# Performance work log

Hardware: AMD Instinct MI355X
Metric: run time of the kernel (lower is better)

The kernel has to match this reference:

```python
import jax, jax.numpy as jnp
import numpy as np

B, H, W, C = 32, 256, 256, 3
KH, KW, F = 5, 5, 8


def setup_inputs() -> dict:
    key = jax.random.key(0)
    k1, k2 = jax.random.split(key)
    x = jax.random.normal(k1, (B, H, W, C), dtype=jnp.float32)
    # learned structuring elements, shape (KH, KW, C, F) per build()
    kernel = jax.random.normal(k2, (KH, KW, C, F), dtype=jnp.float32) * 0.1
    return {"x": x, "kernel": kernel}


def _max_of_erosions(x, kernel):
    # tf.nn.erosion2d semantics: out[b,y,x,c] = min_{dy,dx} in[b, y+dy-pt, x+dx-pl, c]
    #                                               - kernel[KH-1-dy, KW-1-dx, c]
    # (erosion = -dilation(-x, reversed kernel)); then channel-max per filter.
    Bq, Hq, Wq, Cq = x.shape
    kh, kw, _, nf = kernel.shape
    pad_h, pad_w = kh - 1, kw - 1          # stride 1, rate 1, SAME padding
    pt, pl = pad_h // 2, pad_w // 2
    xp = jnp.pad(x, ((0, 0), (pt, pad_h - pt), (pl, pad_w - pl), (0, 0)),
                 constant_values=jnp.inf)   # +inf is identity for min
    kflip = kernel[::-1, ::-1]              # reflected structuring element
    ero = None                              # running min over window taps
    for dy in range(kh):                    # small fixed 5x5 tap loop
        for dx in range(kw):
            win = xp[:, dy:dy + Hq, dx:dx + Wq, :]          # [B,H,W,C]
            cand = win[..., None] - kflip[dy, dx]           # [B,H,W,C,F]
            ero = cand if ero is None else jnp.minimum(ero, cand)
    return jnp.max(ero, axis=3)             # channel max -> [B,H,W,F]


def reference(x, kernel):
    return _max_of_erosions(x, kernel)
```

## Files before the change

### kernel.cpp

```cpp
#include <hip/hip_runtime.h>
#include <math.h>


typedef _Float16 h2 __attribute__((ext_vector_type(2)));

static __device__ __forceinline__ h2 cvt_pk(float a, float b) {
    return __builtin_bit_cast(h2, __builtin_amdgcn_cvt_pkrtz(a, b));
}
static __device__ __forceinline__ h2 u2h(unsigned u) {
    return __builtin_bit_cast(h2, u);
}

#define Hq 256
#define RSTR 396
#define TILE_H2 (8 * RSTR)
#define INF2 0x7C007C00u

__global__ __launch_bounds__(256) void maxero_np(
    const float* __restrict__ x,
    const float* __restrict__ kern,
    float* __restrict__ out)
{
    __shared__ __align__(16) h2 xlds[TILE_H2];
    __shared__ __align__(16) h2 klds[25 * 12];

    const int tid = threadIdx.x;
    const int bI  = blockIdx.x;
    const int b   = bI >> 6;
    const int h0  = (bI & 63) << 2;

    for (int i = tid; i < 300; i += 256) {
        int tap = i / 12;
        int rem = i - tap * 12;
        int c = rem >> 2, fp = rem & 3;
        int dy = tap / 5, dx = tap - dy * 5;
        const float* kp = kern + (((4 - dy) * 5 + (4 - dx)) * 24) + c * 8 + fp * 2;
        klds[i] = cvt_pk(kp[0], kp[1]);
    }

    const float* xb = x + (size_t)b * (Hq * 256 * 3);
    #pragma unroll
    for (int k = 0; k < 6; ++k) {
        int chunk = tid + k * 256;
        int rr    = chunk / 192;
        int off   = (chunk - rr * 192) * 4;
        int r     = h0 - 2 + rr;
        bool rv   = (unsigned)r < (unsigned)Hq;
        int rc    = min(max(r, 0), Hq - 1);
        const float4 v = *reinterpret_cast<const float4*>(xb + rc * 768 + off);
        h2* d = &xlds[rr * RSTR + 9 + (off >> 1)];
        d[0] = rv ? cvt_pk(v.x, v.y) : u2h(INF2);
        d[1] = rv ? cvt_pk(v.z, v.w) : u2h(INF2);
    }
    if (tid < 96) {
        int rr = tid / 12, p = tid - rr * 12;
        xlds[rr * RSTR + (p < 9 ? p : 384 + p)] = u2h(INF2);
    }
    __syncthreads();

    const int hrow = tid >> 6;
    const int w0   = (tid & 63) << 2;

    h2 ero[4][3][4];
    #pragma unroll
    for (int p = 0; p < 4; ++p)
        #pragma unroll
        for (int c = 0; c < 3; ++c)
            #pragma unroll
            for (int fp = 0; fp < 4; ++fp)
                ero[p][c][fp] = u2h(INF2);

    #pragma unroll
    for (int dy = 0; dy < 5; ++dy) {
        const uint2* rp = reinterpret_cast<const uint2*>(
            &xlds[(hrow + dy) * RSTR + 6 + ((3 * w0) >> 1)]);
        unsigned nat[12];
        #pragma unroll
        for (int q = 0; q < 6; ++q) {
            uint2 t = rp[q];
            nat[q * 2 + 0] = t.x;
            nat[q * 2 + 1] = t.y;
        }
        #pragma unroll
        for (int dx = 0; dx < 5; ++dx) {
            const uint4* kk = reinterpret_cast<const uint4*>(&klds[(dy * 5 + dx) * 12]);
            uint4 k0 = kk[0], k1 = kk[1], k2 = kk[2];
            const unsigned kf[12] = { k0.x, k0.y, k0.z, k0.w,
                                      k1.x, k1.y, k1.z, k1.w,
                                      k2.x, k2.y, k2.z, k2.w };
            #pragma unroll
            for (int p = 0; p < 4; ++p)
                #pragma unroll
                for (int c = 0; c < 3; ++c) {
                    const int e = (p + dx) * 3 + c;
                    _Float16 s = u2h(nat[e >> 1])[e & 1];
                    h2 xx = { s, s };
                    #pragma unroll
                    for (int fp = 0; fp < 4; ++fp) {
                        h2 cand = xx - u2h(kf[c * 4 + fp]);
                        ero[p][c][fp] = __builtin_elementwise_min(ero[p][c][fp], cand);
                    }
                }
        }
    }

    const size_t rowbase = (size_t)b * 65536 + (size_t)(h0 + hrow) * 256 + w0;
    #pragma unroll
    for (int p = 0; p < 4; ++p) {
        float of[8];
        #pragma unroll
        for (int fp = 0; fp < 4; ++fp) {
            h2 m = __builtin_elementwise_max(
                       __builtin_elementwise_max(ero[p][0][fp], ero[p][1][fp]),
                       ero[p][2][fp]);
            of[fp * 2 + 0] = (float)m[0];
            of[fp * 2 + 1] = (float)m[1];
        }
        float* op = out + (rowbase + p) * 8;
        reinterpret_cast<float4*>(op)[0] = make_float4(of[0], of[1], of[2], of[3]);
        reinterpret_cast<float4*>(op)[1] = make_float4(of[4], of[5], of[6], of[7]);
    }
}

extern "C" void kernel_launch(void* const* d_in, const int* in_sizes, int n_in,
                              void* d_out, int out_size, void* d_ws, size_t ws_size,
                              hipStream_t stream) {
    const float* x    = (const float*)d_in[0];
    const float* kern = (const float*)d_in[1];
    float* out        = (float*)d_out;
    maxero_np<<<2048, 256, 0, stream>>>(x, kern, out);
}
```

Before: 53.97 us.

## Store input tile channel-planar so packed halves hold adjacent pixels

The shared-memory input tile moves from interleaved NHWC to per-channel planes, so each packed fp16 pair holds two neighbouring pixels of one channel. The kernel weights are now stored broadcast into both halves. Odd-offset pixel pairs are built with alignbit, so no per-element extract and broadcast is needed. This drops the scalar-to-vector splat work from the inner min loop. The cost is more LDS for the weights and a more involved global-to-LDS transpose.

```diff
diff --git a/kernel.cpp b/kernel.cpp
--- a/kernel.cpp
+++ b/kernel.cpp
@@ -12,114 +12,125 @@
 }
 
 #define Hq 256
-#define RSTR 396
-#define TILE_H2 (8 * RSTR)
+#define RST 132
+#define PST (8 * RST)
+#define TILE_H2 (3 * PST)
 #define INF2 0x7C007C00u
 
-__global__ __launch_bounds__(256) void maxero_np(
+__global__ __launch_bounds__(256) void maxero_pp(
     const float* __restrict__ x,
     const float* __restrict__ kern,
     float* __restrict__ out)
 {
-    __shared__ __align__(16) h2 xlds[TILE_H2];
-    __shared__ __align__(16) h2 klds[25 * 12];
+    __shared__ __align__(16) h2 xp[TILE_H2];
+    __shared__ __align__(16) h2 kd[600];
 
     const int tid = threadIdx.x;
     const int bI  = blockIdx.x;
     const int b   = bI >> 6;
     const int h0  = (bI & 63) << 2;
 
-    for (int i = tid; i < 300; i += 256) {
-        int tap = i / 12;
-        int rem = i - tap * 12;
-        int c = rem >> 2, fp = rem & 3;
+    for (int i = tid; i < 600; i += 256) {
+        int tap = i / 24, rem = i - tap * 24;
+        int c = rem >> 3, f = rem & 7;
         int dy = tap / 5, dx = tap - dy * 5;
-        const float* kp = kern + (((4 - dy) * 5 + (4 - dx)) * 24) + c * 8 + fp * 2;
-        klds[i] = cvt_pk(kp[0], kp[1]);
+        float v = kern[((4 - dy) * 5 + (4 - dx)) * 24 + c * 8 + f];
+        kd[i] = cvt_pk(v, v);
     }
 
     const float* xb = x + (size_t)b * (Hq * 256 * 3);
     #pragma unroll
-    for (int k = 0; k < 6; ++k) {
-        int chunk = tid + k * 256;
-        int rr    = chunk / 192;
-        int off   = (chunk - rr * 192) * 4;
-        int r     = h0 - 2 + rr;
-        bool rv   = (unsigned)r < (unsigned)Hq;
-        int rc    = min(max(r, 0), Hq - 1);
-        const float4 v = *reinterpret_cast<const float4*>(xb + rc * 768 + off);
-        h2* d = &xlds[rr * RSTR + 9 + (off >> 1)];
-        d[0] = rv ? cvt_pk(v.x, v.y) : u2h(INF2);
-        d[1] = rv ? cvt_pk(v.z, v.w) : u2h(INF2);
+    for (int k = 0; k < 2; ++k) {
+        int g   = tid + k * 256;
+        int rr  = g >> 6;
+        int pg  = g & 63;
+        int r   = h0 - 2 + rr;
+        bool rv = (unsigned)r < (unsigned)Hq;
+        int rc  = min(max(r, 0), Hq - 1);
+        const float4* gp = reinterpret_cast<const float4*>(xb + rc * 768 + pg * 12);
+        float4 v0 = gp[0], v1 = gp[1], v2 = gp[2];
+        const float fv[12] = { v0.x, v0.y, v0.z, v0.w,
+                               v1.x, v1.y, v1.z, v1.w,
+                               v2.x, v2.y, v2.z, v2.w };
+        int base = rr * RST + 2 * pg + 1;
+        #pragma unroll
+        for (int c = 0; c < 3; ++c) {
+            xp[c * PST + base + 0] = rv ? cvt_pk(fv[c],     fv[3 + c]) : u2h(INF2);
+            xp[c * PST + base + 1] = rv ? cvt_pk(fv[6 + c], fv[9 + c]) : u2h(INF2);
+        }
     }
-    if (tid < 96) {
-        int rr = tid / 12, p = tid - rr * 12;
-        xlds[rr * RSTR + (p < 9 ? p : 384 + p)] = u2h(INF2);
+    if (tid < 48) {
+        int c = tid >> 4, rem = tid & 15;
+        int rr = rem >> 1, side = rem & 1;
+        xp[c * PST + rr * RST + (side ? 129 : 0)] = u2h(INF2);
     }
     __syncthreads();
 
     const int hrow = tid >> 6;
     const int w0   = (tid & 63) << 2;
 
-    h2 ero[4][3][4];
+    h2 e01[3][8], e23[3][8];
     #pragma unroll
-    for (int p = 0; p < 4; ++p)
+    for (int c = 0; c < 3; ++c)
         #pragma unroll
-        for (int c = 0; c < 3; ++c)
-            #pragma unroll
-            for (int fp = 0; fp < 4; ++fp)
-                ero[p][c][fp] = u2h(INF2);
+        for (int f = 0; f < 8; ++f) {
+            e01[c][f] = u2h(INF2);
+            e23[c][f] = u2h(INF2);
+        }
 
     #pragma unroll
     for (int dy = 0; dy < 5; ++dy) {
-        const uint2* rp = reinterpret_cast<const uint2*>(
-            &xlds[(hrow + dy) * RSTR + 6 + ((3 * w0) >> 1)]);
-        unsigned nat[12];
+        unsigned a[3][4], mis[3][3];
         #pragma unroll
-        for (int q = 0; q < 6; ++q) {
-            uint2 t = rp[q];
-            nat[q * 2 + 0] = t.x;
-            nat[q * 2 + 1] = t.y;
+        for (int c = 0; c < 3; ++c) {
+            const h2* xr = &xp[c * PST + (hrow + dy) * RST + (w0 >> 1)];
+            uint2 u0 = *reinterpret_cast<const uint2*>(xr);
+            uint2 u1 = *reinterpret_cast<const uint2*>(xr + 2);
+            a[c][0] = u0.x; a[c][1] = u0.y; a[c][2] = u1.x; a[c][3] = u1.y;
+            mis[c][0] = __builtin_amdgcn_alignbit(a[c][1], a[c][0], 16);
+            mis[c][1] = __builtin_amdgcn_alignbit(a[c][2], a[c][1], 16);
+            mis[c][2] = __builtin_amdgcn_alignbit(a[c][3], a[c][2], 16);
         }
         #pragma unroll
         for (int dx = 0; dx < 5; ++dx) {
-            const uint4* kk = reinterpret_cast<const uint4*>(&klds[(dy * 5 + dx) * 12]);
-            uint4 k0 = kk[0], k1 = kk[1], k2 = kk[2];
-            const unsigned kf[12] = { k0.x, k0.y, k0.z, k0.w,
-                                      k1.x, k1.y, k1.z, k1.w,
-                                      k2.x, k2.y, k2.z, k2.w };
             #pragma unroll
-            for (int p = 0; p < 4; ++p)
+            for (int c = 0; c < 3; ++c) {
+                h2 p01 = u2h((dx & 1) ? mis[c][dx >> 1]       : a[c][dx >> 1]);
+                h2 p23 = u2h((dx & 1) ? mis[c][(dx >> 1) + 1] : a[c][(dx >> 1) + 1]);
+                const uint4* kk = reinterpret_cast<const uint4*>(
+                    &kd[(dy * 5 + dx) * 24 + c * 8]);
+                uint4 k0 = kk[0], k1 = kk[1];
+                const unsigned kf[8] = { k0.x, k0.y, k0.z, k0.w,
+                                         k1.x, k1.y, k1.z, k1.w };
                 #pragma unroll
-                for (int c = 0; c < 3; ++c) {
-                    const int e = (p + dx) * 3 + c;
-                    _Float16 s = u2h(nat[e >> 1])[e & 1];
-                    h2 xx = { s, s };
-                    #pragma unroll
-                    for (int fp = 0; fp < 4; ++fp) {
-                        h2 cand = xx - u2h(kf[c * 4 + fp]);
-                        ero[p][c][fp] = __builtin_elementwise_min(ero[p][c][fp], cand);
-                    }
+                for (int f = 0; f < 8; ++f) {
+                    e01[c][f] = __builtin_elementwise_min(e01[c][f], p01 - u2h(kf[f]));
+                    e23[c][f] = __builtin_elementwise_min(e23[c][f], p23 - u2h(kf[f]));
                 }
+            }
         }
     }
 
+    float o0[8], o1[8], o2[8], o3[8];
+    #pragma unroll
+    for (int f = 0; f < 8; ++f) {
+        h2 m01 = __builtin_elementwise_max(
+                     __builtin_elementwise_max(e01[0][f], e01[1][f]), e01[2][f]);
+        h2 m23 = __builtin_elementwise_max(
+                     __builtin_elementwise_max(e23[0][f], e23[1][f]), e23[2][f]);
+        o0[f] = (float)m01[0]; o1[f] = (float)m01[1];
+        o2[f] = (float)m23[0]; o3[f] = (float)m23[1];
+    }
     const size_t rowbase = (size_t)b * 65536 + (size_t)(h0 + hrow) * 256 + w0;
-    #pragma unroll
-    for (int p = 0; p < 4; ++p) {
-        float of[8];
-        #pragma unroll
-        for (int fp = 0; fp < 4; ++fp) {
-            h2 m = __builtin_elementwise_max(
-                       __builtin_elementwise_max(ero[p][0][fp], ero[p][1][fp]),
-                       ero[p][2][fp]);
-            of[fp * 2 + 0] = (float)m[0];
-            of[fp * 2 + 1] = (float)m[1];
-        }
-        float* op = out + (rowbase + p) * 8;
-        reinterpret_cast<float4*>(op)[0] = make_float4(of[0], of[1], of[2], of[3]);
-        reinterpret_cast<float4*>(op)[1] = make_float4(of[4], of[5], of[6], of[7]);
-    }
+    float* op = out + rowbase * 8;
+    reinterpret_cast<float4*>(op)[0] = make_float4(o0[0], o0[1], o0[2], o0[3]);
+    reinterpret_cast<float4*>(op)[1] = make_float4(o0[4], o0[5], o0[6], o0[7]);
+    reinterpret_cast<float4*>(op)[2] = make_float4(o1[0], o1[1], o1[2], o1[3]);
+    reinterpret_cast<float4*>(op)[3] = make_float4(o1[4], o1[5], o1[6], o1[7]);
+    reinterpret_cast<float4*>(op)[4] = make_float4(o2[0], o2[1], o2[2], o2[3]);
+    reinterpret_cast<float4*>(op)[5] = make_float4(o2[4], o2[5], o2[6], o2[7]);
+    reinterpret_cast<float4*>(op)[6] = make_float4(o3[0], o3[1], o3[2], o3[3]);
+    reinterpret_cast<float4*>(op)[7] = make_float4(o3[4], o3[5], o3[6], o3[7]);
 }
 
 extern "C" void kernel_launch(void* const* d_in, const int* in_sizes, int n_in,
@@ -128,5 +139,5 @@
     const float* x    = (const float*)d_in[0];
     const float* kern = (const float*)d_in[1];
     float* out        = (float*)d_out;
-    maxero_np<<<2048, 256, 0, stream>>>(x, kern, out);
+    maxero_pp<<<2048, 256, 0, stream>>>(x, kern, out);
 }
```

Result: faster. 51.41 us (-4.7%).
